# Kernel optimization log

Hardware: AMD Instinct MI355X
Metric: run time of the kernel (lower is better)

Reference implementation:

```python
import jax, jax.numpy as jnp
import numpy as np

E, S, L = 32, 64, 32          # episodes, steps, max_comm_len
H, D_IN, C = 512, 1536, 64    # hidden_size, pvrnn_mtrnn_size + 2*hidden, comm_shape


def setup_inputs() -> dict:
    key = jax.random.key(0)
    ks = jax.random.split(key, 12)
    sd = 0.02
    inp = {
        "h_w_action": jax.random.normal(ks[0], (E, S, D_IN), jnp.float32),
        "Wx": jax.random.normal(ks[1], (D_IN, H), jnp.float32) * sd,
        "bx": jnp.zeros((H,), jnp.float32),
        "Wh": jax.random.normal(ks[2], (H, H), jnp.float32) * sd,
        "bh": jnp.zeros((H,), jnp.float32),
        "prelu_a": jnp.float32(0.25),  # nn.PReLU default single-param init
        "Wout": jax.random.normal(ks[3], (H, C), jnp.float32) * sd,
        "bout": jnp.zeros((C,), jnp.float32),
    }
    for i, k in enumerate([1, 3, 5, 7]):
        inp[f"conv_w{k}"] = jax.random.normal(ks[4 + i], (H // 4, H, k), jnp.float32) * sd
        inp[f"conv_b{k}"] = jnp.zeros((H // 4,), jnp.float32)
    return inp


def _conv1d_reflect(x, w, b):
    # x: (N, Cin, L), w: (Cout, Cin, K) -> 'same' conv with reflect padding
    k = w.shape[-1]
    p = (k - 1) // 2
    if p > 0:
        x = jnp.pad(x, ((0, 0), (0, 0), (p, p)), mode="reflect")
    y = jax.lax.conv_general_dilated(
        x, w, window_strides=(1,), padding="VALID",
        dimension_numbers=("NCW", "OIW", "NCW"))
    return y + b[None, :, None]


def _forward(h_w_action, Wx, bx, Wh, bh,
             conv_w1, conv_b1, conv_w3, conv_b3,
             conv_w5, conv_b5, conv_w7, conv_b7,
             prelu_a, Wout, bout):
    e, s, d = h_w_action.shape
    x = h_w_action.reshape(e * s, d)                 # (N, D_IN)
    xw = x @ Wx + bx                                  # precompute input drive once

    # MTRNN with time_constant=1 -> h_new = tanh(Wx x + Wh h); same x every step
    def step(h, _):
        h = jnp.tanh(xw + h @ Wh + bh)
        return h, h

    h0 = jnp.zeros((e * s, H), h_w_action.dtype)
    _, hs = jax.lax.scan(step, h0, None, length=L)   # (L, N, H)
    comm_h = jnp.transpose(hs, (1, 2, 0))            # (N, H, L) channels-first

    # Ted_Conv1d: 4 parallel convs (kernels 1,3,5,7), concat on channels
    y = jnp.concatenate([
        _conv1d_reflect(comm_h, conv_w1, conv_b1),
        _conv1d_reflect(comm_h, conv_w3, conv_b3),
        _conv1d_reflect(comm_h, conv_w5, conv_b5),
        _conv1d_reflect(comm_h, conv_w7, conv_b7),
    ], axis=1)                                        # (N, H, L)
    y = jnp.where(y >= 0, y, prelu_a * y)             # PReLU; dropout is eval-mode identity

    y = jnp.transpose(y, (0, 2, 1)).reshape(e, s, L, H)
    comm_pred = y @ Wout + bout                       # (E, S, L, C)

    # create_comm_mask: keep tokens up to and including the first end token (argmax == 0)
    is_end = jnp.argmax(comm_pred, axis=-1) == 0      # (E, S, L)
    before_first_end = (jnp.cumsum(is_end.astype(jnp.int32), axis=-1)
                        - is_end.astype(jnp.int32)) == 0
    mask = before_first_end.astype(comm_pred.dtype)
    return comm_pred * mask[..., None]


def reference(h_w_action, Wx, bx, Wh, bh,
              conv_w1, conv_b1, conv_w3, conv_b3,
              conv_w5, conv_b5, conv_w7, conv_b7,
              prelu_a, Wout, bout):
    return _forward(h_w_action, Wx, bx, Wh, bh,
                    conv_w1, conv_b1, conv_w3, conv_b3,
                    conv_w5, conv_b5, conv_w7, conv_b7,
                    prelu_a, Wout, bout)
```

## Files before the change

### kernel.cpp

```cpp
#include <hip/hip_runtime.h>
#include <cmath>

#define LSEQ 32
#define HID  512
#define DIN  1536
#define CCH  64
#define NROW 2048
#define NL   65536

typedef _Float16 f16;
typedef _Float16 f16x8 __attribute__((ext_vector_type(8)));
typedef float    f32x4 __attribute__((ext_vector_type(4)));
typedef unsigned long long u64;

__device__ __forceinline__ float fast_tanh(float x) {
  float e = __expf(2.0f * x);
  return 1.0f - 2.0f * __builtin_amdgcn_rcpf(e + 1.0f);
}

__device__ __forceinline__ int offA(int r, int b) {
  return (r << 6) + (b ^ (((r >> 1) & 3) << 4));
}
__device__ __forceinline__ int offB(int r, int b) {
  return (r << 10) + (b ^ ((r & 7) << 4));
}

__global__ void pack_wc_kernel(const float* __restrict__ w1, const float* __restrict__ w3,
                               const float* __restrict__ w5, const float* __restrict__ w7,
                               f16* __restrict__ Wc_t) {
  int idx = blockIdx.x * 256 + threadIdx.x;
  if (idx >= 7 * 512 * 512) return;
  int k   = idx & 511;
  int c   = (idx >> 9) & 511;
  int dli = idx >> 18;
  int dl  = dli - 3;
  int g   = c >> 7, cg = c & 127;
  int K   = 2 * g + 1;
  int kk  = dl + g;
  float v = 0.f;
  if (kk >= 0 && kk < K) {
    const float* w = (g == 0) ? w1 : (g == 1) ? w3 : (g == 2) ? w5 : w7;
    v = w[(cg * 512 + k) * K + kk];
  }
  Wc_t[idx] = (f16)v;
}

__global__ void pack_misc_kernel(const float* __restrict__ Wh, const float* __restrict__ Wout,
                                 const float* __restrict__ Wx,
                                 f16* __restrict__ Wh_t, f16* __restrict__ Wout_t,
                                 f16* __restrict__ Wx_t) {
  int idx = blockIdx.x * 256 + threadIdx.x;
  if (idx < 512 * 512) {
    int n = idx >> 9, k = idx & 511;
    Wh_t[idx] = (f16)Wh[k * 512 + n];
  } else if (idx < 512 * 512 + 64 * 512) {
    int j = idx - 512 * 512;
    int c = j >> 9, k = j & 511;
    Wout_t[j] = (f16)Wout[k * 64 + c];
  } else {
    int j = idx - (512 * 512 + 64 * 512);
    if (j < 512 * 1536) {
      int n = j / 1536, k = j - n * 1536;
      Wx_t[j] = (f16)Wx[k * 512 + n];
    }
  }
}

__global__ void pack_x_kernel(const float* __restrict__ x,
                              f16* __restrict__ x_hi, f16* __restrict__ x_lo) {
  int idx = blockIdx.x * 256 + threadIdx.x;
  float v = x[idx];
  f16 hi = (f16)v;
  x_hi[idx] = hi;
  x_lo[idx] = (f16)(v - (float)hi);
}

__global__ __launch_bounds__(256) void xw_mfma_kernel(
    const f16* __restrict__ x_hi, const f16* __restrict__ x_lo,
    const f16* __restrict__ Wx_t, const float* __restrict__ bx,
    float* __restrict__ xw)
{
  __shared__ __align__(16) char Ah[2][4096], Al[2][4096], Bt[2][8192];
  const int tid = threadIdx.x, lane = tid & 63, wave = tid >> 6;
  const int r0 = blockIdx.x * 64, c0 = blockIdx.y * 128;
  const int wr = (wave >> 1) * 32, wc = (wave & 1) * 64;
  const int q = lane >> 4, ln = lane & 15, qb = q << 4;

  const int arow = tid & 63, acb = (tid >> 6) << 4;
  const char* srcAh = (const char*)(x_hi + (size_t)(r0 + arow) * DIN) + acb;
  const char* srcAl = (const char*)(x_lo + (size_t)(r0 + arow) * DIN) + acb;
  const int wAo = offA(arow, acb);
  const int brow = tid & 127, bcb = (tid >> 7) << 5;
  const char* srcB = (const char*)(Wx_t + (size_t)(c0 + brow) * DIN) + bcb;
  const int wB0 = offA(brow, bcb), wB1 = offA(brow, bcb + 16);

  *(int4*)(Ah[0] + wAo) = *(const int4*)(srcAh);
  *(int4*)(Al[0] + wAo) = *(const int4*)(srcAl);
  *(int4*)(Bt[0] + wB0) = *(const int4*)(srcB);
  *(int4*)(Bt[0] + wB1) = *(const int4*)(srcB + 16);
  __syncthreads();

  f32x4 acc[2][4] = {};
  for (int kk = 0; kk < 48; ++kk) {
    const int buf = kk & 1;
    int4 ra, rl, rb0, rb1;
    if (kk < 47) {
      ra  = *(const int4*)(srcAh + (kk + 1) * 64);
      rl  = *(const int4*)(srcAl + (kk + 1) * 64);
      rb0 = *(const int4*)(srcB  + (kk + 1) * 64);
      rb1 = *(const int4*)(srcB  + (kk + 1) * 64 + 16);
    }
    f16x8 bf[4];
#pragma unroll
    for (int n = 0; n < 4; ++n)
      bf[n] = *(const f16x8*)(Bt[buf] + offA(wc + n * 16 + ln, qb));
#pragma unroll
    for (int m = 0; m < 2; ++m) {
      f16x8 ah = *(const f16x8*)(Ah[buf] + offA(wr + m * 16 + ln, qb));
      f16x8 al = *(const f16x8*)(Al[buf] + offA(wr + m * 16 + ln, qb));
#pragma unroll
      for (int n = 0; n < 4; ++n) {
        acc[m][n] = __builtin_amdgcn_mfma_f32_16x16x32_f16(ah, bf[n], acc[m][n], 0, 0, 0);
        acc[m][n] = __builtin_amdgcn_mfma_f32_16x16x32_f16(al, bf[n], acc[m][n], 0, 0, 0);
      }
    }
    if (kk < 47) {
      *(int4*)(Ah[buf ^ 1] + wAo) = ra;
      *(int4*)(Al[buf ^ 1] + wAo) = rl;
      *(int4*)(Bt[buf ^ 1] + wB0) = rb0;
      *(int4*)(Bt[buf ^ 1] + wB1) = rb1;
      __syncthreads();
    }
  }
#pragma unroll
  for (int m = 0; m < 2; ++m)
#pragma unroll
    for (int i = 0; i < 4; ++i) {
      const int R = r0 + wr + m * 16 + q * 4 + i;
#pragma unroll
      for (int n = 0; n < 4; ++n) {
        const int C = c0 + wc + n * 16 + ln;
        xw[(size_t)R * HID + C] = acc[m][n][i] + bx[C];
      }
    }
}

__global__ __launch_bounds__(512, 2) void rnn_all_kernel(
    f16* __restrict__ hs_hi, const f16* __restrict__ Wh_t,
    const float* __restrict__ xw, const float* __restrict__ bh)
{
  __shared__ __align__(16) char Hs[2][2][16384];
  const int tid = threadIdx.x, lane = tid & 63, w = tid >> 6;
  const int n0 = blockIdx.x * 16;
  const int q = lane >> 4, ln = lane & 15;
  const int cbase = w * 64;

  float xwbh[4][4];
  {
    const float* xwrow = xw + (size_t)(n0 + ln) * HID + cbase + (q << 2);
    const float* bhp   = bh + cbase + (q << 2);
#pragma unroll
    for (int nt = 0; nt < 4; ++nt) {
      float4 xv = *(const float4*)(xwrow + nt * 16);
      float4 bv = *(const float4*)(bhp + nt * 16);
      xwbh[nt][0] = xv.x + bv.x;
      xwbh[nt][1] = xv.y + bv.y;
      xwbh[nt][2] = xv.z + bv.z;
      xwbh[nt][3] = xv.w + bv.w;
    }
  }

  f16x8 wh[4][16];
#pragma unroll
  for (int nt = 0; nt < 4; ++nt) {
    const char* pA = (const char*)Wh_t + ((size_t)(cbase + nt * 16 + ln) << 10) + (q << 4);
#pragma unroll
    for (int ks = 0; ks < 16; ++ks)
      wh[nt][ks] = *(const f16x8*)(pA + (ks << 6));
  }

  int wo[4];
#pragma unroll
  for (int nt = 0; nt < 4; ++nt) {
    const int ksp  = w * 2 + (nt >> 1);
    const int kgrp = ((nt & 1) << 1) | (q >> 1);
    wo[nt] = (ksp << 10) | (kgrp << 8) | ((ln ^ (ksp & 7)) << 4) | ((q & 1) << 3);
  }

  const int cks = lane >> 2;
  const int src0 = (cks << 10) | ((lane & 3) << 8) | ((w ^ (cks & 7)) << 4);
  const int src1 = (cks << 10) | ((lane & 3) << 8) | (((w + 8) ^ (cks & 7)) << 4);
  char* gdst0 = (char*)hs_hi + (((size_t)(n0 + w) * LSEQ) << 10) + (lane << 4);
  char* gdst1 = (char*)hs_hi + (((size_t)(n0 + w + 8) * LSEQ) << 10) + (lane << 4);

  for (int ts = 0; ts < LSEQ; ++ts) {
    f32x4 acc[4] = {};
    if (ts > 0) {
      const char* Hb = Hs[(ts - 1) & 1][0];
#pragma unroll
      for (int ks = 0; ks < 16; ++ks) {
        const int ro = (ks << 10) | ((lane ^ (ks & 7)) << 4);
        f16x8 bhf = *(const f16x8*)(Hb + ro);
        f16x8 blf = *(const f16x8*)(Hb + 16384 + ro);
#pragma unroll
        for (int nt = 0; nt < 4; ++nt) {
          acc[nt] = __builtin_amdgcn_mfma_f32_16x16x32_f16(wh[nt][ks], bhf, acc[nt], 0, 0, 0);
          acc[nt] = __builtin_amdgcn_mfma_f32_16x16x32_f16(wh[nt][ks], blf, acc[nt], 0, 0, 0);
        }
      }
    }
    char* Hw = Hs[ts & 1][0];
#pragma unroll
    for (int nt = 0; nt < 4; ++nt) {
      union { u64 u; f16 h[4]; } H, L;
#pragma unroll
      for (int i = 0; i < 4; ++i) {
        float v = fast_tanh(acc[nt][i] + xwbh[nt][i]);
        f16 hi = (f16)v;
        H.h[i] = hi;
        L.h[i] = (f16)(v - (float)hi);
      }
      *(u64*)(Hw + wo[nt])         = H.u;
      *(u64*)(Hw + 16384 + wo[nt]) = L.u;
    }
    __syncthreads();
    *(int4*)(gdst0 + (ts << 10)) = *(const int4*)(Hw + src0);
    *(int4*)(gdst1 + (ts << 10)) = *(const int4*)(Hw + src1);
  }
}

__global__ __launch_bounds__(256) void conv_mfma_kernel(
    const f16* __restrict__ hs_hi, const f16* __restrict__ Wc_t,
    const float* __restrict__ b1, const float* __restrict__ b3,
    const float* __restrict__ b5, const float* __restrict__ b7,
    const float* __restrict__ prelu_a, f16* __restrict__ y)
{
  __shared__ __align__(16) char Atile[2][8192];
  __shared__ __align__(16) char Btile[2][8192];
  const int tid = threadIdx.x, lane = tid & 63, wave = tid >> 6;
  const int r0 = blockIdx.x * 128;
  const int g  = blockIdx.y;
  const int taps = 2 * g + 1;
  const int wr = (wave >> 1) * 64, wc = (wave & 1) * 64;
  const int q = lane >> 4, ln = lane & 15;

  const int srow = tid >> 1;
  const int sb   = (tid & 1) << 5;
  const char* srcA = (const char*)(hs_hi + (size_t)(r0 + srow) * HID) + sb;
  const int wA0 = offA(srow, sb), wA1 = offA(srow, sb + 16);

  *(int4*)(Atile[0] + wA0) = *(const int4*)(srcA);
  *(int4*)(Atile[0] + wA1) = *(const int4*)(srcA + 16);
  {
    const char* p = (const char*)(Wc_t + ((size_t)(0 - g + 3) * HID + (g * 128 + srow)) * HID) + sb;
    *(int4*)(Btile[0] + wA0) = *(const int4*)(p);
    *(int4*)(Btile[0] + wA1) = *(const int4*)(p + 16);
  }
  __syncthreads();

  f32x4 acc[4][4] = {};
  int cur = 0, curA = 0;
  for (int kk = 0; kk < 16; ++kk) {
    for (int tp = 0; tp < taps; ++tp) {
      const bool lastPhase = (kk == 15) && (tp == taps - 1);
      const int nkk = (tp == taps - 1) ? kk + 1 : kk;
      const int ntp = (tp == taps - 1) ? 0 : tp + 1;
      int4 rb0, rb1, ra0, ra1;
      bool stA = false;
      if (!lastPhase) {
        const char* p = (const char*)(Wc_t + ((size_t)(ntp - g + 3) * HID + (g * 128 + srow)) * HID + nkk * 32) + sb;
        rb0 = *(const int4*)(p);
        rb1 = *(const int4*)(p + 16);
        if (ntp == 0) {
          stA = true;
          ra0 = *(const int4*)(srcA + nkk * 64);
          ra1 = *(const int4*)(srcA + nkk * 64 + 16);
        }
      }
      const int dl = tp - g;
      f16x8 af[4], bf[4];
#pragma unroll
      for (int m = 0; m < 4; ++m) {
        const int lr = wr + m * 16 + ln;
        int tt = (lr & 31) + dl;
        tt = (tt < 0) ? -tt : ((tt > 31) ? 62 - tt : tt);
        af[m] = *(const f16x8*)(Atile[curA] + offA((lr & ~31) | tt, q << 4));
      }
#pragma unroll
      for (int n = 0; n < 4; ++n)
        bf[n] = *(const f16x8*)(Btile[cur] + offA(wc + n * 16 + ln, q << 4));
      __builtin_amdgcn_s_setprio(1);
#pragma unroll
      for (int m = 0; m < 4; ++m)
#pragma unroll
        for (int n = 0; n < 4; ++n)
          acc[m][n] = __builtin_amdgcn_mfma_f32_16x16x32_f16(af[m], bf[n], acc[m][n], 0, 0, 0);
      __builtin_amdgcn_s_setprio(0);
      if (!lastPhase) {
        *(int4*)(Btile[cur ^ 1] + wA0) = rb0;
        *(int4*)(Btile[cur ^ 1] + wA1) = rb1;
        if (stA) {
          *(int4*)(Atile[curA ^ 1] + wA0) = ra0;
          *(int4*)(Atile[curA ^ 1] + wA1) = ra1;
        }
        __syncthreads();
        cur ^= 1;
        if (stA) curA ^= 1;
      }
    }
  }

  const float pa = *prelu_a;
  const float* bg = (g == 0) ? b1 : (g == 1) ? b3 : (g == 2) ? b5 : b7;
#pragma unroll
  for (int m = 0; m < 4; ++m)
#pragma unroll
    for (int i = 0; i < 4; ++i) {
      const int R = r0 + wr + m * 16 + q * 4 + i;
#pragma unroll
      for (int n = 0; n < 4; ++n) {
        const int cg = wc + n * 16 + ln;
        float v = acc[m][n][i] + bg[cg];
        v = (v >= 0.f) ? v : pa * v;
        y[(size_t)R * HID + g * 128 + cg] = (f16)v;
      }
    }
}

__global__ __launch_bounds__(256) void out_mfma_kernel(
    const f16* __restrict__ y, const f16* __restrict__ Wout_t,
    const float* __restrict__ bout, float* __restrict__ out)
{
  __shared__ __align__(16) char Bl[65536];
  __shared__ __align__(16) char Atile[2][8192];
  const int tid = threadIdx.x, lane = tid & 63, wave = tid >> 6;
  const int r0 = blockIdx.x * 128;
  const int q = lane >> 4, ln = lane & 15;

  {
    const int rr = tid >> 2;
    const char* src = (const char*)(Wout_t + (size_t)rr * HID);
#pragma unroll
    for (int i = 0; i < 16; ++i) {
      const int cb = (((tid & 3) + (i << 2)) << 4);
      *(int4*)(Bl + offB(rr, cb)) = *(const int4*)(src + cb);
    }
  }
  const int srow = tid >> 1, sb = (tid & 1) << 5;
  const char* srcA = (const char*)(y + (size_t)(r0 + srow) * HID) + sb;
  const int wA0 = offA(srow, sb), wA1 = offA(srow, sb + 16);
  *(int4*)(Atile[0] + wA0) = *(const int4*)(srcA);
  *(int4*)(Atile[0] + wA1) = *(const int4*)(srcA + 16);
  __syncthreads();

  f32x4 acc[2][4] = {};
#pragma unroll
  for (int ks = 0; ks < 16; ++ks) {
    const int buf = ks & 1;
    int4 na0, na1;
    if (ks < 15) {
      na0 = *(const int4*)(srcA + (ks + 1) * 64);
      na1 = *(const int4*)(srcA + (ks + 1) * 64 + 16);
    }
    f16x8 af[2], bf[4];
#pragma unroll
    for (int m = 0; m < 2; ++m)
      af[m] = *(const f16x8*)(Atile[buf] + offA(wave * 32 + m * 16 + ln, q << 4));
#pragma unroll
    for (int n = 0; n < 4; ++n)
      bf[n] = *(const f16x8*)(Bl + offB(n * 16 + ln, (ks << 6) + (q << 4)));
#pragma unroll
    for (int m = 0; m < 2; ++m)
#pragma unroll
      for (int n = 0; n < 4; ++n)
        acc[m][n] = __builtin_amdgcn_mfma_f32_16x16x32_f16(af[m], bf[n], acc[m][n], 0, 0, 0);
    if (ks < 15) {
      *(int4*)(Atile[buf ^ 1] + wA0) = na0;
      *(int4*)(Atile[buf ^ 1] + wA1) = na1;
      __syncthreads();
    }
  }
#pragma unroll
  for (int m = 0; m < 2; ++m)
#pragma unroll
    for (int i = 0; i < 4; ++i) {
      const int R = r0 + wave * 32 + m * 16 + q * 4 + i;
#pragma unroll
      for (int n = 0; n < 4; ++n) {
        const int C = n * 16 + ln;
        out[(size_t)R * CCH + C] = acc[m][n][i] + bout[C];
      }
    }
}

__global__ void mask_kernel(float* __restrict__ out) {
  const int row  = blockIdx.x;
  const int lane = threadIdx.x;
  float* base = out + (long)row * (LSEQ * CCH);
  int ended = 0;
  for (int l = 0; l < LSEQ; ++l) {
    float v = base[l * CCH + lane];
    float mv = v; int mi = lane;
#pragma unroll
    for (int off = 32; off > 0; off >>= 1) {
      float ov = __shfl_xor(mv, off);
      int   oi = __shfl_xor(mi, off);
      if (ov > mv || (ov == mv && oi < mi)) { mv = ov; mi = oi; }
    }
    if (ended) base[l * CCH + lane] = 0.f;
    ended |= (mi == 0);
  }
}

extern "C" void kernel_launch(void* const* d_in, const int* in_sizes, int n_in,
                              void* d_out, int out_size, void* d_ws, size_t ws_size,
                              hipStream_t stream) {
  const float* x    = (const float*)d_in[0];
  const float* Wx   = (const float*)d_in[1];
  const float* bx   = (const float*)d_in[2];
  const float* Wh   = (const float*)d_in[3];
  const float* bh   = (const float*)d_in[4];
  const float* pa   = (const float*)d_in[5];
  const float* Wout = (const float*)d_in[6];
  const float* bout = (const float*)d_in[7];
  const float* cw1  = (const float*)d_in[8];
  const float* cb1  = (const float*)d_in[9];
  const float* cw3  = (const float*)d_in[10];
  const float* cb3  = (const float*)d_in[11];
  const float* cw5  = (const float*)d_in[12];
  const float* cb5  = (const float*)d_in[13];
  const float* cw7  = (const float*)d_in[14];
  const float* cb7  = (const float*)d_in[15];
  float* out = (float*)d_out;

  char* ws = (char*)d_ws;
  f16*   hs_hi  = (f16*)(ws);
  f16*   Wout_t = (f16*)(ws + 67108864);
  f16*   Wc_t   = (f16*)(ws + 67174400);
  char*  big    = ws + 70844416;
  float* xw     = (float*)(big);
  f16*   Wh_t   = (f16*)(big + 4194304);
  f16*   x_hi   = (f16*)(big + 4718592);
  f16*   x_lo   = (f16*)(big + 11010048);
  f16*   Wx_t   = (f16*)(big + 17301504);
  f16*   y      = (f16*)(big);

  pack_wc_kernel<<<7 * 512 * 512 / 256, 256, 0, stream>>>(cw1, cw3, cw5, cw7, Wc_t);
  pack_misc_kernel<<<4224, 256, 0, stream>>>(Wh, Wout, Wx, Wh_t, Wout_t, Wx_t);
  pack_x_kernel<<<NROW * DIN / 256, 256, 0, stream>>>(x, x_hi, x_lo);

  xw_mfma_kernel<<<dim3(NROW / 64, HID / 128), 256, 0, stream>>>(x_hi, x_lo, Wx_t, bx, xw);

  rnn_all_kernel<<<NROW / 16, 512, 0, stream>>>(hs_hi, Wh_t, xw, bh);

  conv_mfma_kernel<<<dim3(NL / 128, 4), 256, 0, stream>>>(
      hs_hi, Wc_t, cb1, cb3, cb5, cb7, pa, y);

  out_mfma_kernel<<<NL / 128, 256, 0, stream>>>(y, Wout_t, bout, out);

  mask_kernel<<<NROW, 64, 0, stream>>>(out);
}
```

Measured before the change: 441.1 us.

## Template conv kernel by tap count, double K-step, stream half of Wh

The conv kernel becomes a template over the kernel-size group, so the tap loop is fully unrolled. Each pipeline stage now covers a K chunk of 64 instead of 32, which halves the number of barriers and staging rounds, at the cost of twice the shared memory per block. In the RNN kernel only half of the Wh fragments stay in registers; the other half is streamed from global memory with a one-step prefetch. This lowers register pressure but adds global or cache loads on the serial recurrence path.

```diff
diff --git a/kernel.cpp b/kernel.cpp
--- a/kernel.cpp
+++ b/kernel.cpp
@@ -170,14 +170,16 @@
     }
   }
 
-  f16x8 wh[4][16];
-#pragma unroll
-  for (int nt = 0; nt < 4; ++nt) {
+  f16x8 wh01[2][16];
+#pragma unroll
+  for (int nt = 0; nt < 2; ++nt) {
     const char* pA = (const char*)Wh_t + ((size_t)(cbase + nt * 16 + ln) << 10) + (q << 4);
 #pragma unroll
     for (int ks = 0; ks < 16; ++ks)
-      wh[nt][ks] = *(const f16x8*)(pA + (ks << 6));
-  }
+      wh01[nt][ks] = *(const f16x8*)(pA + (ks << 6));
+  }
+  const char* pA2 = (const char*)Wh_t + ((size_t)(cbase + 32 + ln) << 10) + (q << 4);
+  const char* pA3 = (const char*)Wh_t + ((size_t)(cbase + 48 + ln) << 10) + (q << 4);
 
   int wo[4];
 #pragma unroll
@@ -197,16 +199,26 @@
     f32x4 acc[4] = {};
     if (ts > 0) {
       const char* Hb = Hs[(ts - 1) & 1][0];
+      f16x8 c2 = *(const f16x8*)(pA2);
+      f16x8 c3 = *(const f16x8*)(pA3);
 #pragma unroll
       for (int ks = 0; ks < 16; ++ks) {
+        f16x8 t2 = c2, t3 = c3;
+        if (ks < 15) {
+          c2 = *(const f16x8*)(pA2 + ((ks + 1) << 6));
+          c3 = *(const f16x8*)(pA3 + ((ks + 1) << 6));
+        }
         const int ro = (ks << 10) | ((lane ^ (ks & 7)) << 4);
         f16x8 bhf = *(const f16x8*)(Hb + ro);
         f16x8 blf = *(const f16x8*)(Hb + 16384 + ro);
-#pragma unroll
-        for (int nt = 0; nt < 4; ++nt) {
-          acc[nt] = __builtin_amdgcn_mfma_f32_16x16x32_f16(wh[nt][ks], bhf, acc[nt], 0, 0, 0);
-          acc[nt] = __builtin_amdgcn_mfma_f32_16x16x32_f16(wh[nt][ks], blf, acc[nt], 0, 0, 0);
-        }
+        acc[0] = __builtin_amdgcn_mfma_f32_16x16x32_f16(wh01[0][ks], bhf, acc[0], 0, 0, 0);
+        acc[0] = __builtin_amdgcn_mfma_f32_16x16x32_f16(wh01[0][ks], blf, acc[0], 0, 0, 0);
+        acc[1] = __builtin_amdgcn_mfma_f32_16x16x32_f16(wh01[1][ks], bhf, acc[1], 0, 0, 0);
+        acc[1] = __builtin_amdgcn_mfma_f32_16x16x32_f16(wh01[1][ks], blf, acc[1], 0, 0, 0);
+        acc[2] = __builtin_amdgcn_mfma_f32_16x16x32_f16(t2, bhf, acc[2], 0, 0, 0);
+        acc[2] = __builtin_amdgcn_mfma_f32_16x16x32_f16(t2, blf, acc[2], 0, 0, 0);
+        acc[3] = __builtin_amdgcn_mfma_f32_16x16x32_f16(t3, bhf, acc[3], 0, 0, 0);
+        acc[3] = __builtin_amdgcn_mfma_f32_16x16x32_f16(t3, blf, acc[3], 0, 0, 0);
       }
     }
     char* Hw = Hs[ts & 1][0];
@@ -227,6 +239,119 @@
     *(int4*)(gdst0 + (ts << 10)) = *(const int4*)(Hw + src0);
     *(int4*)(gdst1 + (ts << 10)) = *(const int4*)(Hw + src1);
   }
+}
+
+template<int G>
+__device__ __forceinline__ void conv_body(
+    const f16* __restrict__ hs_hi, const f16* __restrict__ Wc_t,
+    const float* __restrict__ bg, float pa, f16* __restrict__ y,
+    int rb, int tid, char* Ab, char* Bb)
+{
+  constexpr int TAPS = 2 * G + 1;
+  const int lane = tid & 63, wave = tid >> 6;
+  const int r0 = rb * 128;
+  const int wr = (wave >> 1) * 64, wc = (wave & 1) * 64;
+  const int q = lane >> 4, ln = lane & 15, qb = q << 4;
+
+  const int srow = tid >> 1, sb = (tid & 1) << 5;
+  const char* srcA = (const char*)(hs_hi + (size_t)(r0 + srow) * HID);
+  const char* srcB = (const char*)(Wc_t + (size_t)(G * 128 + srow) * HID);
+  const int wA0 = offA(srow, sb), wA1 = offA(srow, sb + 16);
+
+#pragma unroll
+  for (int h = 0; h < 2; ++h) {
+    *(int4*)(Ab + h * 8192 + wA0) = *(const int4*)(srcA + h * 64 + sb);
+    *(int4*)(Ab + h * 8192 + wA1) = *(const int4*)(srcA + h * 64 + sb + 16);
+    const char* pb = srcB + ((size_t)(3 - G) << 19) + h * 64 + sb;
+    *(int4*)(Bb + h * 8192 + wA0) = *(const int4*)(pb);
+    *(int4*)(Bb + h * 8192 + wA1) = *(const int4*)(pb + 16);
+  }
+  __syncthreads();
+
+  f32x4 acc[4][4] = {};
+  int cur = 0, curA = 0;
+  for (int kk = 0; kk < 8; ++kk) {
+#pragma unroll
+    for (int tp = 0; tp < TAPS; ++tp) {
+      const bool last = (kk == 7) && (tp == TAPS - 1);
+      const int nkk = (tp == TAPS - 1) ? kk + 1 : kk;
+      const int ntp = (tp == TAPS - 1) ? 0 : tp + 1;
+      const bool stA = (tp == TAPS - 1) && !last;
+      int4 rb0[2], rb1[2], ra0[2], ra1[2];
+      if (!last) {
+#pragma unroll
+        for (int h = 0; h < 2; ++h) {
+          const char* pb = srcB + ((size_t)(ntp - G + 3) << 19) + nkk * 128 + h * 64 + sb;
+          rb0[h] = *(const int4*)(pb);
+          rb1[h] = *(const int4*)(pb + 16);
+        }
+        if (stA) {
+#pragma unroll
+          for (int h = 0; h < 2; ++h) {
+            ra0[h] = *(const int4*)(srcA + nkk * 128 + h * 64 + sb);
+            ra1[h] = *(const int4*)(srcA + nkk * 128 + h * 64 + sb + 16);
+          }
+        }
+      }
+      const int dl = tp - G;
+      int rrow[4];
+#pragma unroll
+      for (int m = 0; m < 4; ++m) {
+        const int lr = wr + m * 16 + ln;
+        int tt = (lr & 31) + dl;
+        tt = (tt < 0) ? -tt : ((tt > 31) ? 62 - tt : tt);
+        rrow[m] = (lr & ~31) | tt;
+      }
+      __builtin_amdgcn_s_setprio(1);
+#pragma unroll
+      for (int h = 0; h < 2; ++h) {
+        f16x8 af[4], bf[4];
+#pragma unroll
+        for (int m = 0; m < 4; ++m)
+          af[m] = *(const f16x8*)(Ab + curA * 16384 + h * 8192 + offA(rrow[m], qb));
+#pragma unroll
+        for (int n = 0; n < 4; ++n)
+          bf[n] = *(const f16x8*)(Bb + cur * 16384 + h * 8192 + offA(wc + n * 16 + ln, qb));
+#pragma unroll
+        for (int m = 0; m < 4; ++m)
+#pragma unroll
+          for (int n = 0; n < 4; ++n)
+            acc[m][n] = __builtin_amdgcn_mfma_f32_16x16x32_f16(af[m], bf[n], acc[m][n], 0, 0, 0);
+      }
+      __builtin_amdgcn_s_setprio(0);
+      if (!last) {
+#pragma unroll
+        for (int h = 0; h < 2; ++h) {
+          *(int4*)(Bb + (cur ^ 1) * 16384 + h * 8192 + wA0) = rb0[h];
+          *(int4*)(Bb + (cur ^ 1) * 16384 + h * 8192 + wA1) = rb1[h];
+        }
+        if (stA) {
+#pragma unroll
+          for (int h = 0; h < 2; ++h) {
+            *(int4*)(Ab + (curA ^ 1) * 16384 + h * 8192 + wA0) = ra0[h];
+            *(int4*)(Ab + (curA ^ 1) * 16384 + h * 8192 + wA1) = ra1[h];
+          }
+        }
+        __syncthreads();
+        cur ^= 1;
+        if (stA) curA ^= 1;
+      }
+    }
+  }
+
+#pragma unroll
+  for (int m = 0; m < 4; ++m)
+#pragma unroll
+    for (int i = 0; i < 4; ++i) {
+      const int R = r0 + wr + m * 16 + q * 4 + i;
+#pragma unroll
+      for (int n = 0; n < 4; ++n) {
+        const int cg = wc + n * 16 + ln;
+        float v = acc[m][n][i] + bg[cg];
+        v = (v >= 0.f) ? v : pa * v;
+        y[(size_t)R * HID + G * 128 + cg] = (f16)v;
+      }
+    }
 }
 
 __global__ __launch_bounds__(256) void conv_mfma_kernel(
@@ -235,96 +360,17 @@
     const float* __restrict__ b5, const float* __restrict__ b7,
     const float* __restrict__ prelu_a, f16* __restrict__ y)
 {
-  __shared__ __align__(16) char Atile[2][8192];
-  __shared__ __align__(16) char Btile[2][8192];
-  const int tid = threadIdx.x, lane = tid & 63, wave = tid >> 6;
-  const int r0 = blockIdx.x * 128;
-  const int g  = blockIdx.y;
-  const int taps = 2 * g + 1;
-  const int wr = (wave >> 1) * 64, wc = (wave & 1) * 64;
-  const int q = lane >> 4, ln = lane & 15;
-
-  const int srow = tid >> 1;
-  const int sb   = (tid & 1) << 5;
-  const char* srcA = (const char*)(hs_hi + (size_t)(r0 + srow) * HID) + sb;
-  const int wA0 = offA(srow, sb), wA1 = offA(srow, sb + 16);
-
-  *(int4*)(Atile[0] + wA0) = *(const int4*)(srcA);
-  *(int4*)(Atile[0] + wA1) = *(const int4*)(srcA + 16);
-  {
-    const char* p = (const char*)(Wc_t + ((size_t)(0 - g + 3) * HID + (g * 128 + srow)) * HID) + sb;
-    *(int4*)(Btile[0] + wA0) = *(const int4*)(p);
-    *(int4*)(Btile[0] + wA1) = *(const int4*)(p + 16);
-  }
-  __syncthreads();
-
-  f32x4 acc[4][4] = {};
-  int cur = 0, curA = 0;
-  for (int kk = 0; kk < 16; ++kk) {
-    for (int tp = 0; tp < taps; ++tp) {
-      const bool lastPhase = (kk == 15) && (tp == taps - 1);
-      const int nkk = (tp == taps - 1) ? kk + 1 : kk;
-      const int ntp = (tp == taps - 1) ? 0 : tp + 1;
-      int4 rb0, rb1, ra0, ra1;
-      bool stA = false;
-      if (!lastPhase) {
-        const char* p = (const char*)(Wc_t + ((size_t)(ntp - g + 3) * HID + (g * 128 + srow)) * HID + nkk * 32) + sb;
-        rb0 = *(const int4*)(p);
-        rb1 = *(const int4*)(p + 16);
-        if (ntp == 0) {
-          stA = true;
-          ra0 = *(const int4*)(srcA + nkk * 64);
-          ra1 = *(const int4*)(srcA + nkk * 64 + 16);
-        }
-      }
-      const int dl = tp - g;
-      f16x8 af[4], bf[4];
-#pragma unroll
-      for (int m = 0; m < 4; ++m) {
-        const int lr = wr + m * 16 + ln;
-        int tt = (lr & 31) + dl;
-        tt = (tt < 0) ? -tt : ((tt > 31) ? 62 - tt : tt);
-        af[m] = *(const f16x8*)(Atile[curA] + offA((lr & ~31) | tt, q << 4));
-      }
-#pragma unroll
-      for (int n = 0; n < 4; ++n)
-        bf[n] = *(const f16x8*)(Btile[cur] + offA(wc + n * 16 + ln, q << 4));
-      __builtin_amdgcn_s_setprio(1);
-#pragma unroll
-      for (int m = 0; m < 4; ++m)
-#pragma unroll
-        for (int n = 0; n < 4; ++n)
-          acc[m][n] = __builtin_amdgcn_mfma_f32_16x16x32_f16(af[m], bf[n], acc[m][n], 0, 0, 0);
-      __builtin_amdgcn_s_setprio(0);
-      if (!lastPhase) {
-        *(int4*)(Btile[cur ^ 1] + wA0) = rb0;
-        *(int4*)(Btile[cur ^ 1] + wA1) = rb1;
-        if (stA) {
-          *(int4*)(Atile[curA ^ 1] + wA0) = ra0;
-          *(int4*)(Atile[curA ^ 1] + wA1) = ra1;
-        }
-        __syncthreads();
-        cur ^= 1;
-        if (stA) curA ^= 1;
-      }
-    }
-  }
-
+  __shared__ __align__(16) char At[2][2][8192];
+  __shared__ __align__(16) char Bt[2][2][8192];
+  const int g = blockIdx.y, rb = blockIdx.x;
+  const int tid = threadIdx.x;
   const float pa = *prelu_a;
-  const float* bg = (g == 0) ? b1 : (g == 1) ? b3 : (g == 2) ? b5 : b7;
-#pragma unroll
-  for (int m = 0; m < 4; ++m)
-#pragma unroll
-    for (int i = 0; i < 4; ++i) {
-      const int R = r0 + wr + m * 16 + q * 4 + i;
-#pragma unroll
-      for (int n = 0; n < 4; ++n) {
-        const int cg = wc + n * 16 + ln;
-        float v = acc[m][n][i] + bg[cg];
-        v = (v >= 0.f) ? v : pa * v;
-        y[(size_t)R * HID + g * 128 + cg] = (f16)v;
-      }
-    }
+  switch (g) {
+    case 0: conv_body<0>(hs_hi, Wc_t, b1, pa, y, rb, tid, &At[0][0][0], &Bt[0][0][0]); break;
+    case 1: conv_body<1>(hs_hi, Wc_t, b3, pa, y, rb, tid, &At[0][0][0], &Bt[0][0][0]); break;
+    case 2: conv_body<2>(hs_hi, Wc_t, b5, pa, y, rb, tid, &At[0][0][0], &Bt[0][0][0]); break;
+    default: conv_body<3>(hs_hi, Wc_t, b7, pa, y, rb, tid, &At[0][0][0], &Bt[0][0][0]); break;
+  }
 }
 
 __global__ __launch_bounds__(256) void out_mfma_kernel(
```

Measured after the change: 663.3 us. +50.4%, slower.
